# Performance work log

Measured on AMD Instinct MI355X. Metric: run time of the kernel, lower is better.

The kernel has to match this reference:

```python
import jax, jax.numpy as jnp
import numpy as np
import math

D_MODEL = 1024
N_HEADS = 16
D_K = D_MODEL // N_HEADS
B, S = 4, 2048


def setup_inputs() -> dict:
    key = jax.random.key(0)
    ks = jax.random.split(key, 11)
    std = 1.0 / math.sqrt(D_MODEL)
    inp = {
        "query": jax.random.normal(ks[0], (B, S, D_MODEL), dtype=jnp.float32),
        "key_in": jax.random.normal(ks[1], (B, S, D_MODEL), dtype=jnp.float32),
        "value": jax.random.normal(ks[2], (B, S, D_MODEL), dtype=jnp.float32),
        "Wq": jax.random.normal(ks[3], (D_MODEL, D_MODEL), dtype=jnp.float32) * std,
        "bq": jnp.zeros((D_MODEL,), dtype=jnp.float32),
        "Wk": jax.random.normal(ks[4], (D_MODEL, D_MODEL), dtype=jnp.float32) * std,
        "bk": jnp.zeros((D_MODEL,), dtype=jnp.float32),
        "Wv": jax.random.normal(ks[5], (D_MODEL, D_MODEL), dtype=jnp.float32) * std,
        "bv": jnp.zeros((D_MODEL,), dtype=jnp.float32),
        "Wo": jax.random.normal(ks[6], (D_MODEL, D_MODEL), dtype=jnp.float32) * std,
        "bo": jnp.zeros((D_MODEL,), dtype=jnp.float32),
    }
    return inp


def reference(query, key_in, value, Wq, bq, Wk, bk, Wv, bv, Wo, bo):
    b, s, _ = query.shape
    scale = math.sqrt(D_K)
    # projections: nn.Linear computes x @ W.T + b
    Q = (query @ Wq.T + bq).reshape(b, s, N_HEADS, D_K).transpose(0, 2, 1, 3)
    K = (key_in @ Wk.T + bk).reshape(b, s, N_HEADS, D_K).transpose(0, 2, 1, 3)
    V = (value @ Wv.T + bv).reshape(b, s, N_HEADS, D_K).transpose(0, 2, 1, 3)
    # [b, h, s, s]
    scores = jnp.einsum("bhqd,bhkd->bhqk", Q, K) / scale
    causal = jnp.tril(jnp.ones((s, s), dtype=bool))
    scores = jnp.where(causal[None, None, :, :], scores, jnp.float32(-1e9))
    attn = jax.nn.softmax(scores, axis=-1)
    out = jnp.einsum("bhqk,bhkd->bhqd", attn, V)
    out = out.transpose(0, 2, 1, 3).reshape(b, s, D_MODEL)
    return out @ Wo.T + bo
```

## Files before the change

### kernel.cpp

```cpp
#include <hip/hip_runtime.h>
#include <hip/hip_bf16.h>
#include <cstdint>

#define DM   1024
#define NH   16
#define DKK  64
#define BB   4
#define SS   2048

typedef __attribute__((ext_vector_type(8)))  short short8;
typedef __attribute__((ext_vector_type(4)))  float f32x4;
typedef __attribute__((ext_vector_type(16))) float f32x16;

__device__ __forceinline__ unsigned short f2bf(float f) {
    union { float f; uint32_t u; } v; v.f = f;
    uint32_t u = v.u;
    uint32_t r = (u + 0x7FFFu + ((u >> 16) & 1u)) >> 16;
    return (unsigned short)r;
}

#define GLL(src, dst) __builtin_amdgcn_global_load_lds(                      \
        (__attribute__((address_space(1))) void*)(src),                      \
        (__attribute__((address_space(3))) void*)(dst), 16, 0, 0)

__global__ void cvt_all(const float* __restrict__ q, const float* __restrict__ k,
                        const float* __restrict__ v,
                        const float* __restrict__ wq, const float* __restrict__ wk,
                        const float* __restrict__ wv, const float* __restrict__ wo,
                        unsigned short* __restrict__ dact, unsigned short* __restrict__ dw)
{
    int i = blockIdx.x * 256 + threadIdx.x;
    const float* s;
    unsigned short* d;
    if (i < 3145728) {
        int a = i >> 20, r = i & 1048575;
        int j = r >> 7, kb = r & 127;
        int kbs = (kb & ~7) | ((kb ^ j) & 7);
        s = (a == 0 ? q : a == 1 ? k : v) + (size_t)j * 1024 + kbs * 8;
        d = dact + ((size_t)a << 23) + (size_t)j * 1024 + kb * 8;
    } else {
        int t = i - 3145728;
        int a = t >> 17, r = t & 131071;
        int j = r >> 7, kb = r & 127;
        int kbs = (kb & ~7) | ((kb ^ j) & 7);
        s = (a == 0 ? wq : a == 1 ? wk : a == 2 ? wv : wo) + (size_t)j * 1024 + kbs * 8;
        d = dw + ((size_t)a << 20) + (size_t)j * 1024 + kb * 8;
    }
    float4 f0 = *(const float4*)(s);
    float4 f1 = *(const float4*)(s + 4);
    union { uint32_t u[4]; short8 s8; } c;
    asm("v_cvt_pk_bf16_f32 %0, %1, %2" : "=v"(c.u[0]) : "v"(f0.x), "v"(f0.y));
    asm("v_cvt_pk_bf16_f32 %0, %1, %2" : "=v"(c.u[1]) : "v"(f0.z), "v"(f0.w));
    asm("v_cvt_pk_bf16_f32 %0, %1, %2" : "=v"(c.u[2]) : "v"(f1.x), "v"(f1.y));
    asm("v_cvt_pk_bf16_f32 %0, %1, %2" : "=v"(c.u[3]) : "v"(f1.z), "v"(f1.w));
    *(short8*)d = c.s8;
}

__global__ __launch_bounds__(512, 2) void gemm_qkv(
        const unsigned short* __restrict__ Act,
        const unsigned short* __restrict__ Wq, const unsigned short* __restrict__ Wk,
        const unsigned short* __restrict__ Wv,
        const float* __restrict__ bq, const float* __restrict__ bk, const float* __restrict__ bv,
        unsigned short* __restrict__ Qo, unsigned short* __restrict__ Ko,
        unsigned short* __restrict__ Vo, const float qscale)
{
    const int orig = blockIdx.x;
    const int wid  = (orig & 7) * 48 + (orig >> 3);
    const int z    = wid >> 7;
    const int r    = wid & 127;
    const int brow = (r >> 2) * 256;
    const int bcol = (r & 3) * 256;

    const unsigned short* A  = Act + ((size_t)z << 23);
    const unsigned short* Bw = (z == 0) ? Wq : (z == 1) ? Wk : Wv;
    const float* bias        = (z == 0) ? bq : (z == 1) ? bk : bv;

    __shared__ __align__(16) unsigned short lA[2][2][8192];
    __shared__ __align__(16) unsigned short lB[2][2][8192];

    const int tid = threadIdx.x;
    const int w = tid >> 6, l = tid & 63;
    const int wm = w >> 2, wn = w & 3;
    const int lrow = l & 15, hi = l >> 4;

    const unsigned short* Asrc = A  + (size_t)(brow + (tid >> 3)) * 1024 + (tid & 7) * 8;
    const unsigned short* Bsrc = Bw + (size_t)(bcol + (tid >> 3)) * 1024 + (tid & 7) * 8;

    int axr[2];
    axr[0] = ((hi ^ (lrow & 7)) << 4);
    axr[1] = (((4 + hi) ^ (lrow & 7)) << 4);

    short8 bfr[4][2];
    f32x4 acc[8][4] = {};

#define STG_A(KT, H)                                                                         \
    { GLL(Asrc + (size_t)((H) * 128) * 1024 + (KT) * 64,      &lA[(KT) & 1][H][w * 512]);    \
      GLL(Asrc + (size_t)((H) * 128 + 64) * 1024 + (KT) * 64, &lA[(KT) & 1][H][4096 + w * 512]); }
#define STG_B(KT, H)                                                                         \
    { GLL(Bsrc + (size_t)((H) * 128) * 1024 + (KT) * 64,      &lB[(KT) & 1][H][w * 512]);    \
      GLL(Bsrc + (size_t)((H) * 128 + 64) * 1024 + (KT) * 64, &lB[(KT) & 1][H][4096 + w * 512]); }
#define VM4 asm volatile("s_waitcnt vmcnt(4)" ::: "memory")
#define VM0 asm volatile("s_waitcnt vmcnt(0)" ::: "memory")

#define PH(KT, MQ, READB, STG, WAIT)                                                         \
    {                                                                                        \
        const char* la_ = (const char*)lA[(KT) & 1][wm];                                     \
        const char* lb_ = (const char*)lB[(KT) & 1][wn >> 1];                                \
        if (READB) {                                                                         \
            _Pragma("unroll") for (int n = 0; n < 4; ++n)                                    \
            _Pragma("unroll") for (int kk = 0; kk < 2; ++kk)                                 \
                bfr[n][kk] = *(const short8*)(lb_ + ((wn & 1) * 64 + n * 16 + lrow) * 128 + axr[kk]); \
        }                                                                                    \
        short8 af_[2][2];                                                                    \
        _Pragma("unroll") for (int j = 0; j < 2; ++j)                                        \
        _Pragma("unroll") for (int kk = 0; kk < 2; ++kk)                                     \
            af_[j][kk] = *(const short8*)(la_ + (((MQ) * 2 + j) * 16 + lrow) * 128 + axr[kk]); \
        STG;                                                                                 \
        WAIT;                                                                                \
        __builtin_amdgcn_s_barrier();                                                        \
        asm volatile("s_waitcnt lgkmcnt(0)" ::: "memory");                                   \
        __builtin_amdgcn_sched_barrier(0);                                                   \
        __builtin_amdgcn_s_setprio(1);                                                       \
        _Pragma("unroll") for (int j = 0; j < 2; ++j)                                        \
        _Pragma("unroll") for (int n = 0; n < 4; ++n)                                        \
        _Pragma("unroll") for (int kk = 0; kk < 2; ++kk)                                     \
            acc[(MQ) * 2 + j][n] = __builtin_amdgcn_mfma_f32_16x16x32_bf16(                  \
                af_[j][kk], bfr[n][kk], acc[(MQ) * 2 + j][n], 0, 0, 0);                      \
        __builtin_amdgcn_s_setprio(0);                                                       \
        __builtin_amdgcn_s_barrier();                                                        \
    }

    STG_A(0, 0); STG_A(0, 1); STG_B(0, 0); STG_B(0, 1); STG_B(1, 0); STG_B(1, 1);
    VM4;
    __builtin_amdgcn_s_barrier();

    for (int i = 0; i < 7; ++i) {
        const int kt = 2 * i;
        PH(kt,     0, 1, STG_A(kt + 1, 0), (void)0);
        PH(kt,     1, 0, STG_A(kt + 1, 1), (void)0);
        PH(kt,     2, 0, STG_B(kt + 2, 0), (void)0);
        PH(kt,     3, 0, STG_B(kt + 2, 1), VM4);
        PH(kt + 1, 0, 1, STG_A(kt + 2, 0), (void)0);
        PH(kt + 1, 1, 0, STG_A(kt + 2, 1), (void)0);
        PH(kt + 1, 2, 0, STG_B(kt + 3, 0), (void)0);
        PH(kt + 1, 3, 0, STG_B(kt + 3, 1), VM4);
    }
    PH(14, 0, 1, STG_A(15, 0), (void)0);
    PH(14, 1, 0, STG_A(15, 1), (void)0);
    PH(14, 2, 0, (void)0, (void)0);
    PH(14, 3, 0, (void)0, VM0);
    PH(15, 0, 1, (void)0, (void)0);
    PH(15, 1, 0, (void)0, (void)0);
    PH(15, 2, 0, (void)0, (void)0);
    PH(15, 3, 0, (void)0, (void)0);

#undef PH
#undef STG_A
#undef STG_B

    const float ascale = (z == 0) ? qscale : 1.0f;
#pragma unroll
    for (int m = 0; m < 8; ++m) {
#pragma unroll
        for (int n = 0; n < 4; ++n) {
            const int i0 = brow + wm * 128 + m * 16 + hi * 4;
            const int j  = bcol + wn * 64 + n * 16 + lrow;
            const float bj = bias[j];
            const int hh = j >> 6, d = j & 63;
            if (z < 2) {
                unsigned short* Cb = (z == 0) ? Qo : Ko;
#pragma unroll
                for (int t = 0; t < 4; ++t) {
                    const int i = i0 + t;
                    const int b = i >> 11, s = i & 2047;
                    Cb[(((size_t)(b * NH + hh) * SS) + s) * DKK + d] = f2bf((acc[m][n][t] + bj) * ascale);
                }
            } else {
                const int b = i0 >> 11, s0 = i0 & 2047;
                ushort4 pk;
                pk.x = f2bf(acc[m][n][0] + bj);
                pk.y = f2bf(acc[m][n][1] + bj);
                pk.z = f2bf(acc[m][n][2] + bj);
                pk.w = f2bf(acc[m][n][3] + bj);
                *(ushort4*)(Vo + (((size_t)(b * NH + hh) * DKK) + d) * SS + s0) = pk;
            }
        }
    }
}

__global__ __launch_bounds__(256) void gemm_out(
        const unsigned short* __restrict__ A,
        const unsigned short* __restrict__ Bw,
        const float* __restrict__ bias,
        float* __restrict__ Cout)
{
    const int orig = blockIdx.y * 8 + blockIdx.x;
    const int wid  = (orig & 7) * 64 + (orig >> 3);
    const int brow = (wid >> 3) * 128;
    const int bcol = (wid & 7) * 128;

    __shared__ __align__(16) unsigned short lA[128 * 64];
    __shared__ __align__(16) unsigned short lB[2][128 * 64];

    const int tid = threadIdx.x;
    const int w = tid >> 6, l = tid & 63;
    const int wr = (w >> 1) * 64, wc = (w & 1) * 64;
    const int lrow = l & 15;
    const int hi = l >> 4;
    const int sr = l >> 3, scb = l & 7;

    const unsigned short* aga[4];
    const unsigned short* bga[4];
    int awb[4], lbo[4];
#pragma unroll
    for (int i = 0; i < 4; ++i) {
        const int chunk = w * 4 + i;
        const int r = chunk * 8 + sr;
        aga[i] = A  + (size_t)(brow + r) * 1024 + scb * 8;
        bga[i] = Bw + (size_t)(bcol + r) * 1024 + scb * 8;
        awb[i] = chunk * 1024 + sr * 128 + ((scb ^ sr) << 4);
        lbo[i] = chunk * 512;
    }

    short8 aX[4], aY[4];
    f32x4 acc[4][4] = {};

#pragma unroll
    for (int i = 0; i < 4; ++i) GLL(bga[i], lB[0] + lbo[i]);
#pragma unroll
    for (int i = 0; i < 4; ++i) aX[i] = *(const short8*)(aga[i]);
#pragma unroll
    for (int i = 0; i < 4; ++i) aY[i] = *(const short8*)(aga[i] + 64);

#define OUT_WR(CUR)                                                     \
    _Pragma("unroll")                                                   \
    for (int i = 0; i < 4; ++i)                                         \
        *(short8*)((char*)lA + awb[i]) = CUR[i];

#define OUT_MFMA(LB)                                                                              \
    {                                                                                             \
        const unsigned short* lb = (LB);                                                          \
        __builtin_amdgcn_s_setprio(1);                                                            \
        _Pragma("unroll")                                                                         \
        for (int kk = 0; kk < 2; ++kk) {                                                          \
            short8 af[4], bf[4];                                                                  \
            _Pragma("unroll")                                                                     \
            for (int m = 0; m < 4; ++m) {                                                         \
                const int row = wr + m * 16 + lrow;                                               \
                const int pb = (kk * 4 + hi) ^ (row & 7);                                         \
                af[m] = *(const short8*)((const char*)lA + row * 128 + (pb << 4));                \
            }                                                                                     \
            _Pragma("unroll")                                                                     \
            for (int n = 0; n < 4; ++n) {                                                         \
                const int row = wc + n * 16 + lrow;                                               \
                const int pb = (kk * 4 + hi) ^ (row & 7);                                         \
                bf[n] = *(const short8*)((const char*)lb + row * 128 + (pb << 4));                \
            }                                                                                     \
            _Pragma("unroll")                                                                     \
            for (int m = 0; m < 4; ++m)                                                           \
                _Pragma("unroll")                                                                 \
                for (int n = 0; n < 4; ++n)                                                       \
                    acc[m][n] = __builtin_amdgcn_mfma_f32_16x16x32_bf16(af[m], bf[n], acc[m][n], 0, 0, 0); \
        }                                                                                         \
        __builtin_amdgcn_s_setprio(0);                                                            \
    }

    for (int t = 0; t < 14; t += 2) {
        OUT_WR(aX);
        {
            const int ko = (t + 2) * 64;
#pragma unroll
            for (int i = 0; i < 4; ++i) aX[i] = *(const short8*)(aga[i] + ko);
            const int kb = (t + 1) * 64;
#pragma unroll
            for (int i = 0; i < 4; ++i) GLL(bga[i] + kb, lB[1] + lbo[i]);
        }
        asm volatile("s_waitcnt vmcnt(8) lgkmcnt(0)" ::: "memory");
        __builtin_amdgcn_s_barrier();
        OUT_MFMA(lB[0]);
        asm volatile("" ::: "memory");
        __builtin_amdgcn_s_barrier();

        OUT_WR(aY);
        {
            const int ko = (t + 3) * 64;
#pragma unroll
            for (int i = 0; i < 4; ++i) aY[i] = *(const short8*)(aga[i] + ko);
            const int kb = (t + 2) * 64;
#pragma unroll
            for (int i = 0; i < 4; ++i) GLL(bga[i] + kb, lB[0] + lbo[i]);
        }
        asm volatile("s_waitcnt vmcnt(8) lgkmcnt(0)" ::: "memory");
        __builtin_amdgcn_s_barrier();
        OUT_MFMA(lB[1]);
        asm volatile("" ::: "memory");
        __builtin_amdgcn_s_barrier();
    }
    OUT_WR(aX);
#pragma unroll
    for (int i = 0; i < 4; ++i) GLL(bga[i] + 15 * 64, lB[1] + lbo[i]);
    asm volatile("s_waitcnt vmcnt(4) lgkmcnt(0)" ::: "memory");
    __builtin_amdgcn_s_barrier();
    OUT_MFMA(lB[0]);
    asm volatile("" ::: "memory");
    __builtin_amdgcn_s_barrier();
    OUT_WR(aY);
    asm volatile("s_waitcnt vmcnt(0) lgkmcnt(0)" ::: "memory");
    __builtin_amdgcn_s_barrier();
    OUT_MFMA(lB[1]);

#pragma unroll
    for (int m = 0; m < 4; ++m) {
#pragma unroll
        for (int n = 0; n < 4; ++n) {
            const int i0 = brow + wr + m * 16 + (l >> 4) * 4;
            const int j  = bcol + wc + n * 16 + lrow;
            const float bj = bias[j];
#pragma unroll
            for (int t = 0; t < 4; ++t)
                Cout[(size_t)(i0 + t) * DM + j] = acc[m][n][t] + bj;
        }
    }
#undef OUT_WR
#undef OUT_MFMA
}

__global__ __launch_bounds__(256) void attn_kernel(
        const unsigned short* __restrict__ Q,
        const unsigned short* __restrict__ K,
        const unsigned short* __restrict__ Vt,
        unsigned short* __restrict__ AO)
{
    const int flat = blockIdx.y * 16 + blockIdx.x;
    const int r8 = flat & 7, k8 = flat >> 3;
    const int bh = r8 * 8 + (k8 & 7);
    const int qchunk = 15 - (k8 >> 3);
    const int tid = threadIdx.x;
    const int w = tid >> 6, l = tid & 63;
    const int ln = l & 31, h = l >> 5;
    const int qb = qchunk * 128;
    const int q0w = qb + w * 32;

    __shared__ __align__(16) char lK[2][4096];
    __shared__ __align__(16) char lV[2][4096];

    const unsigned short* Qp = Q  + ((size_t)bh * SS + q0w) * DKK;
    const unsigned short* Kp = K  + (size_t)bh * SS * DKK;
    const unsigned short* Vp = Vt + (size_t)bh * DKK * SS;

    const int srow = tid >> 3, scb = tid & 7;
    const int swb = srow * 128 + ((scb * 16) ^ ((srow & 7) << 4));
    const unsigned short* ksrc = Kp + srow * DKK + scb * 8;
    const int vd = (scb < 4) ? srow : (srow + 32);
    const unsigned short* vsrc = Vp + (size_t)vd * SS + (scb & 3) * 8;

    int ka[4], va[4];
#pragma unroll
    for (int ks = 0; ks < 4; ++ks)
        ka[ks] = ln * 128 + ((ks * 32 + h * 16) ^ ((ln & 7) << 4));
#pragma unroll
    for (int c = 0; c < 4; ++c)
        va[c] = ln * 128 + ((c * 32 + h * 16) ^ ((ln & 7) << 4));

    short8 qf[4];
#pragma unroll
    for (int ks = 0; ks < 4; ++ks)
        qf[ks] = *(const short8*)(Qp + (size_t)ln * DKK + ks * 16 + h * 8);

    f32x16 o0 = {}, o1 = {};
    float lsum = 0.f;

    const int Tc = qb / 32;
    const int NT = Tc + 4;

    auto compute = [&](int t, int buf) {
        const char* kb = lK[buf];
        const char* vb = lV[buf];
        short8 kf[4];
#pragma unroll
        for (int ks = 0; ks < 4; ++ks) kf[ks] = *(const short8*)(kb + ka[ks]);

        f32x16 s = {};
        __builtin_amdgcn_s_setprio(1);
#pragma unroll
        for (int ks = 0; ks < 4; ++ks)
            s = __builtin_amdgcn_mfma_f32_32x32x16_bf16(kf[ks], qf[ks], s, 0, 0, 0);
        __builtin_amdgcn_s_setprio(0);

        const bool diag = (t == Tc + w);
#pragma unroll
        for (int r = 0; r < 16; ++r) {
            float e;
            asm("v_exp_f32 %0, %1" : "=v"(e) : "v"(s[r]));
            if (diag) {
                const int crow = (r & 3) + 8 * (r >> 2) + 4 * h;
                e = (crow > ln) ? 0.f : e;
            }
            s[r] = e;
            lsum += e;
        }

        uint32_t pk[8];
#pragma unroll
        for (int i = 0; i < 8; ++i) {
            uint32_t d;
            asm("v_cvt_pk_bf16_f32 %0, %1, %2" : "=v"(d) : "v"(s[2 * i]), "v"(s[2 * i + 1]));
            pk[i] = d;
        }
        asm("v_permlane32_swap_b32 %0, %1" : "+v"(pk[0]), "+v"(pk[2]));
        asm("v_permlane32_swap_b32 %0, %1" : "+v"(pk[1]), "+v"(pk[3]));
        asm("v_permlane32_swap_b32 %0, %1" : "+v"(pk[4]), "+v"(pk[6]));
        asm("v_permlane32_swap_b32 %0, %1" : "+v"(pk[5]), "+v"(pk[7]));

        union Ux { uint32_t u[4]; short8 s8; } pa0, pa1;
        pa0.u[0] = pk[0]; pa0.u[1] = pk[1]; pa0.u[2] = pk[2]; pa0.u[3] = pk[3];
        pa1.u[0] = pk[4]; pa1.u[1] = pk[5]; pa1.u[2] = pk[6]; pa1.u[3] = pk[7];

        short8 vf00 = *(const short8*)(vb + va[0]);
        short8 vf10 = *(const short8*)(vb + va[1]);
        short8 vf01 = *(const short8*)(vb + va[2]);
        short8 vf11 = *(const short8*)(vb + va[3]);

        __builtin_amdgcn_s_setprio(1);
        o0 = __builtin_amdgcn_mfma_f32_32x32x16_bf16(pa0.s8, vf00, o0, 0, 0, 0);
        o0 = __builtin_amdgcn_mfma_f32_32x32x16_bf16(pa1.s8, vf10, o0, 0, 0, 0);
        o1 = __builtin_amdgcn_mfma_f32_32x32x16_bf16(pa0.s8, vf01, o1, 0, 0, 0);
        o1 = __builtin_amdgcn_mfma_f32_32x32x16_bf16(pa1.s8, vf11, o1, 0, 0, 0);
        __builtin_amdgcn_s_setprio(0);
    };

    short8 kA = *(const short8*)(ksrc);
    short8 vA = *(const short8*)(vsrc);
    *(short8*)(&lK[0][swb]) = kA;
    *(short8*)(&lV[0][swb]) = vA;
    kA = *(const short8*)(ksrc + 2048);
    vA = *(const short8*)(vsrc + 32);
    short8 kB = {}, vB = {};
    __syncthreads();

    int t = 0, buf = 0;
    for (;;) {
        if (t + 2 < NT) {
            kB = *(const short8*)(ksrc + (size_t)(t + 2) * 2048);
            vB = *(const short8*)(vsrc + (size_t)(t + 2) * 32);
        }
        if (t <= Tc + w) compute(t, buf);
        if (t + 1 < NT) {
            *(short8*)(&lK[buf ^ 1][swb]) = kA;
            *(short8*)(&lV[buf ^ 1][swb]) = vA;
        }
        __syncthreads();
        buf ^= 1;
        if (++t == NT) break;

        if (t + 2 < NT) {
            kA = *(const short8*)(ksrc + (size_t)(t + 2) * 2048);
            vA = *(const short8*)(vsrc + (size_t)(t + 2) * 32);
        }
        if (t <= Tc + w) compute(t, buf);
        if (t + 1 < NT) {
            *(short8*)(&lK[buf ^ 1][swb]) = kB;
            *(short8*)(&lV[buf ^ 1][swb]) = vB;
        }
        __syncthreads();
        buf ^= 1;
        if (++t == NT) break;
    }

    lsum += __shfl_xor(lsum, 32, 64);
    const float rcp = 1.0f / lsum;

    const int bb = bh >> 4, hh = bh & 15;
#pragma unroll
    for (int r = 0; r < 16; ++r) {
        const int crow = (r & 3) + 8 * (r >> 2) + 4 * h;
        const float rl = __shfl(rcp, crow, 64);
        const size_t row = (size_t)(bb * SS + q0w + crow) * DM + hh * DKK;
        AO[row + ln]      = f2bf(o0[r] * rl);
        AO[row + 32 + ln] = f2bf(o1[r] * rl);
    }
}

extern "C" void kernel_launch(void* const* d_in, const int* in_sizes, int n_in,
                              void* d_out, int out_size, void* d_ws, size_t ws_size,
                              hipStream_t stream)
{
    const float* query  = (const float*)d_in[0];
    const float* key_in = (const float*)d_in[1];
    const float* value  = (const float*)d_in[2];
    const float* Wq = (const float*)d_in[3];
    const float* bq = (const float*)d_in[4];
    const float* Wk = (const float*)d_in[5];
    const float* bk = (const float*)d_in[6];
    const float* Wv = (const float*)d_in[7];
    const float* bv = (const float*)d_in[8];
    const float* Wo = (const float*)d_in[9];
    const float* bo = (const float*)d_in[10];

    const size_t NACT = (size_t)BB * SS * DM;
    const size_t NWT  = (size_t)DM * DM;

    unsigned short* ws   = (unsigned short*)d_ws;
    unsigned short* actb = ws;
    unsigned short* wqb  = actb + 3 * NACT;
    unsigned short* wkb  = wqb + NWT;
    unsigned short* wvb  = wkb + NWT;
    unsigned short* wob  = wvb + NWT;
    unsigned short* Qb   = wob + NWT;
    unsigned short* Kb   = Qb + NACT;
    unsigned short* Vtb  = Kb + NACT;
    unsigned short* AOb  = Vtb + NACT;

    cvt_all<<<14336, 256, 0, stream>>>(query, key_in, value, Wq, Wk, Wv, Wo, actb, wqb);

    const float QSCALE = 0.125f * 1.44269504088896f;
    gemm_qkv<<<384, 512, 0, stream>>>(actb, wqb, wkb, wvb,
                                      bq, bk, bv, Qb, Kb, Vtb, QSCALE);

    attn_kernel<<<dim3(16, 64), 256, 0, stream>>>(Qb, Kb, Vtb, AOb);

    dim3 gg(DM / 128, (BB * SS) / 128);
    gemm_out<<<gg, 256, 0, stream>>>(AOb, wob, bo, (float*)d_out);
}
```

Measured before the change: 188.2 us.

## Fuse fp32-to-bf16 activation conversion into QKV GEMM A-tile loading

The separate conversion pass over the three fp32 activation tensors is removed. The QKV GEMM now loads fp32 activations into registers, converts them to bf16 in-kernel, and writes them to swizzled LDS, with register double-buffering (rX/rY) across k-steps. This avoids writing and re-reading about 48 MB of bf16 activations in global memory. In exchange it reads twice the A bytes inside the GEMM, adds register pressure and conversion ALU work, and replaces async global-to-LDS loads with register staging.

```diff
diff --git a/kernel.cpp b/kernel.cpp
--- a/kernel.cpp
+++ b/kernel.cpp
@@ -23,29 +23,16 @@
         (__attribute__((address_space(1))) void*)(src),                      \
         (__attribute__((address_space(3))) void*)(dst), 16, 0, 0)
 
-__global__ void cvt_all(const float* __restrict__ q, const float* __restrict__ k,
-                        const float* __restrict__ v,
-                        const float* __restrict__ wq, const float* __restrict__ wk,
-                        const float* __restrict__ wv, const float* __restrict__ wo,
-                        unsigned short* __restrict__ dact, unsigned short* __restrict__ dw)
+__global__ void cvt_w(const float* __restrict__ wq, const float* __restrict__ wk,
+                      const float* __restrict__ wv, const float* __restrict__ wo,
+                      unsigned short* __restrict__ dst)
 {
     int i = blockIdx.x * 256 + threadIdx.x;
-    const float* s;
-    unsigned short* d;
-    if (i < 3145728) {
-        int a = i >> 20, r = i & 1048575;
-        int j = r >> 7, kb = r & 127;
-        int kbs = (kb & ~7) | ((kb ^ j) & 7);
-        s = (a == 0 ? q : a == 1 ? k : v) + (size_t)j * 1024 + kbs * 8;
-        d = dact + ((size_t)a << 23) + (size_t)j * 1024 + kb * 8;
-    } else {
-        int t = i - 3145728;
-        int a = t >> 17, r = t & 131071;
-        int j = r >> 7, kb = r & 127;
-        int kbs = (kb & ~7) | ((kb ^ j) & 7);
-        s = (a == 0 ? wq : a == 1 ? wk : a == 2 ? wv : wo) + (size_t)j * 1024 + kbs * 8;
-        d = dw + ((size_t)a << 20) + (size_t)j * 1024 + kb * 8;
-    }
+    int a = i >> 17;
+    int r = i & 131071;
+    int j = r >> 7, kb = r & 127;
+    int kbs = (kb & ~7) | ((kb ^ j) & 7);
+    const float* s = (a == 0 ? wq : a == 1 ? wk : a == 2 ? wv : wo) + (size_t)j * 1024 + kbs * 8;
     float4 f0 = *(const float4*)(s);
     float4 f1 = *(const float4*)(s + 4);
     union { uint32_t u[4]; short8 s8; } c;
@@ -53,11 +40,11 @@
     asm("v_cvt_pk_bf16_f32 %0, %1, %2" : "=v"(c.u[1]) : "v"(f0.z), "v"(f0.w));
     asm("v_cvt_pk_bf16_f32 %0, %1, %2" : "=v"(c.u[2]) : "v"(f1.x), "v"(f1.y));
     asm("v_cvt_pk_bf16_f32 %0, %1, %2" : "=v"(c.u[3]) : "v"(f1.z), "v"(f1.w));
-    *(short8*)d = c.s8;
+    *(short8*)(dst + ((size_t)a << 20) + (size_t)j * 1024 + kb * 8) = c.s8;
 }
 
 __global__ __launch_bounds__(512, 2) void gemm_qkv(
-        const unsigned short* __restrict__ Act,
+        const float* __restrict__ Aq, const float* __restrict__ Ak, const float* __restrict__ Av,
         const unsigned short* __restrict__ Wq, const unsigned short* __restrict__ Wk,
         const unsigned short* __restrict__ Wv,
         const float* __restrict__ bq, const float* __restrict__ bk, const float* __restrict__ bv,
@@ -71,7 +58,7 @@
     const int brow = (r >> 2) * 256;
     const int bcol = (r & 3) * 256;
 
-    const unsigned short* A  = Act + ((size_t)z << 23);
+    const float* Af          = (z == 0) ? Aq : (z == 1) ? Ak : Av;
     const unsigned short* Bw = (z == 0) ? Wq : (z == 1) ? Wk : Wv;
     const float* bias        = (z == 0) ? bq : (z == 1) ? bk : bv;
 
@@ -83,7 +70,9 @@
     const int wm = w >> 2, wn = w & 3;
     const int lrow = l & 15, hi = l >> 4;
 
-    const unsigned short* Asrc = A  + (size_t)(brow + (tid >> 3)) * 1024 + (tid & 7) * 8;
+    const float* Asrcf = Af + (size_t)(brow + (tid >> 2)) * 1024 + (tid & 3) * 16;
+    const int arow = tid >> 2;
+    const int akb0 = (tid & 3) * 2;
     const unsigned short* Bsrc = Bw + (size_t)(bcol + (tid >> 3)) * 1024 + (tid & 7) * 8;
 
     int axr[2];
@@ -91,18 +80,34 @@
     axr[1] = (((4 + hi) ^ (lrow & 7)) << 4);
 
     short8 bfr[4][2];
+    f32x4 rX[8], rY[8];
     f32x4 acc[8][4] = {};
 
-#define STG_A(KT, H)                                                                         \
-    { GLL(Asrc + (size_t)((H) * 128) * 1024 + (KT) * 64,      &lA[(KT) & 1][H][w * 512]);    \
-      GLL(Asrc + (size_t)((H) * 128 + 64) * 1024 + (KT) * 64, &lA[(KT) & 1][H][4096 + w * 512]); }
+#define LOAD_A(KT, H, R)                                                                     \
+    { _Pragma("unroll") for (int i_ = 0; i_ < 4; ++i_)                                       \
+        R[(H) * 4 + i_] = *(const f32x4*)(Asrcf + (size_t)(H) * 131072 + (KT) * 64 + i_ * 4); }
+
+#define CVT_WR(R, KTW, H)                                                                    \
+    { _Pragma("unroll") for (int b_ = 0; b_ < 2; ++b_) {                                     \
+        union { uint32_t u[4]; short8 s8; } c_;                                              \
+        f32x4 a0_ = R[(H) * 4 + b_ * 2], a1_ = R[(H) * 4 + b_ * 2 + 1];                      \
+        asm("v_cvt_pk_bf16_f32 %0, %1, %2" : "=v"(c_.u[0]) : "v"(a0_[0]), "v"(a0_[1]));      \
+        asm("v_cvt_pk_bf16_f32 %0, %1, %2" : "=v"(c_.u[1]) : "v"(a0_[2]), "v"(a0_[3]));      \
+        asm("v_cvt_pk_bf16_f32 %0, %1, %2" : "=v"(c_.u[2]) : "v"(a1_[0]), "v"(a1_[1]));      \
+        asm("v_cvt_pk_bf16_f32 %0, %1, %2" : "=v"(c_.u[3]) : "v"(a1_[2]), "v"(a1_[3]));      \
+        const int kb_ = akb0 + b_;                                                           \
+        *(short8*)((char*)&lA[(KTW) & 1][H][0] + arow * 128 + ((kb_ << 4) ^ ((arow & 7) << 4))) = c_.s8; \
+    } }
+
 #define STG_B(KT, H)                                                                         \
     { GLL(Bsrc + (size_t)((H) * 128) * 1024 + (KT) * 64,      &lB[(KT) & 1][H][w * 512]);    \
       GLL(Bsrc + (size_t)((H) * 128 + 64) * 1024 + (KT) * 64, &lB[(KT) & 1][H][4096 + w * 512]); }
-#define VM4 asm volatile("s_waitcnt vmcnt(4)" ::: "memory")
-#define VM0 asm volatile("s_waitcnt vmcnt(0)" ::: "memory")
-
-#define PH(KT, MQ, READB, STG, WAIT)                                                         \
+
+#define LGKM0 asm volatile("s_waitcnt lgkmcnt(0)" ::: "memory")
+#define VM12  asm volatile("s_waitcnt vmcnt(12)" ::: "memory")
+#define VM0   asm volatile("s_waitcnt vmcnt(0)" ::: "memory")
+
+#define PH(KT, MQ, READB, STG, CVTWR, WAIT)                                                  \
     {                                                                                        \
         const char* la_ = (const char*)lA[(KT) & 1][wm];                                     \
         const char* lb_ = (const char*)lB[(KT) & 1][wn >> 1];                                \
@@ -116,6 +121,7 @@
         _Pragma("unroll") for (int kk = 0; kk < 2; ++kk)                                     \
             af_[j][kk] = *(const short8*)(la_ + (((MQ) * 2 + j) * 16 + lrow) * 128 + axr[kk]); \
         STG;                                                                                 \
+        CVTWR;                                                                               \
         WAIT;                                                                                \
         __builtin_amdgcn_s_barrier();                                                        \
         asm volatile("s_waitcnt lgkmcnt(0)" ::: "memory");                                   \
@@ -130,33 +136,38 @@
         __builtin_amdgcn_s_barrier();                                                        \
     }
 
-    STG_A(0, 0); STG_A(0, 1); STG_B(0, 0); STG_B(0, 1); STG_B(1, 0); STG_B(1, 1);
-    VM4;
+    LOAD_A(0, 0, rX); LOAD_A(0, 1, rX);
+    STG_B(0, 0); STG_B(0, 1);
+    LOAD_A(1, 0, rY); LOAD_A(1, 1, rY);
+    STG_B(1, 0); STG_B(1, 1);
+    CVT_WR(rX, 0, 0); CVT_WR(rX, 0, 1);
+    asm volatile("s_waitcnt vmcnt(12) lgkmcnt(0)" ::: "memory");
     __builtin_amdgcn_s_barrier();
 
     for (int i = 0; i < 7; ++i) {
         const int kt = 2 * i;
-        PH(kt,     0, 1, STG_A(kt + 1, 0), (void)0);
-        PH(kt,     1, 0, STG_A(kt + 1, 1), (void)0);
-        PH(kt,     2, 0, STG_B(kt + 2, 0), (void)0);
-        PH(kt,     3, 0, STG_B(kt + 2, 1), VM4);
-        PH(kt + 1, 0, 1, STG_A(kt + 2, 0), (void)0);
-        PH(kt + 1, 1, 0, STG_A(kt + 2, 1), (void)0);
-        PH(kt + 1, 2, 0, STG_B(kt + 3, 0), (void)0);
-        PH(kt + 1, 3, 0, STG_B(kt + 3, 1), VM4);
-    }
-    PH(14, 0, 1, STG_A(15, 0), (void)0);
-    PH(14, 1, 0, STG_A(15, 1), (void)0);
-    PH(14, 2, 0, (void)0, (void)0);
-    PH(14, 3, 0, (void)0, VM0);
-    PH(15, 0, 1, (void)0, (void)0);
-    PH(15, 1, 0, (void)0, (void)0);
-    PH(15, 2, 0, (void)0, (void)0);
-    PH(15, 3, 0, (void)0, (void)0);
+        PH(kt,     0, 1, LOAD_A(kt + 2, 0, rX), CVT_WR(rY, kt + 1, 0), LGKM0);
+        PH(kt,     1, 0, LOAD_A(kt + 2, 1, rX), CVT_WR(rY, kt + 1, 1), LGKM0);
+        PH(kt,     2, 0, STG_B(kt + 2, 0),      (void)0,               (void)0);
+        PH(kt,     3, 0, STG_B(kt + 2, 1),      (void)0,               VM12);
+        PH(kt + 1, 0, 1, LOAD_A(kt + 3, 0, rY), CVT_WR(rX, kt + 2, 0), LGKM0);
+        PH(kt + 1, 1, 0, LOAD_A(kt + 3, 1, rY), CVT_WR(rX, kt + 2, 1), LGKM0);
+        PH(kt + 1, 2, 0, STG_B(kt + 3, 0),      (void)0,               (void)0);
+        PH(kt + 1, 3, 0, STG_B(kt + 3, 1),      (void)0,               VM12);
+    }
+    PH(14, 0, 1, (void)0, CVT_WR(rY, 15, 0), LGKM0);
+    PH(14, 1, 0, (void)0, CVT_WR(rY, 15, 1), LGKM0);
+    PH(14, 2, 0, (void)0, (void)0,           (void)0);
+    PH(14, 3, 0, (void)0, (void)0,           VM0);
+    PH(15, 0, 1, (void)0, (void)0,           (void)0);
+    PH(15, 1, 0, (void)0, (void)0,           (void)0);
+    PH(15, 2, 0, (void)0, (void)0,           (void)0);
+    PH(15, 3, 0, (void)0, (void)0,           (void)0);
 
 #undef PH
-#undef STG_A
 #undef STG_B
+#undef LOAD_A
+#undef CVT_WR
 
     const float ascale = (z == 0) ? qscale : 1.0f;
 #pragma unroll
@@ -500,21 +511,20 @@
     const size_t NACT = (size_t)BB * SS * DM;
     const size_t NWT  = (size_t)DM * DM;
 
-    unsigned short* ws   = (unsigned short*)d_ws;
-    unsigned short* actb = ws;
-    unsigned short* wqb  = actb + 3 * NACT;
-    unsigned short* wkb  = wqb + NWT;
-    unsigned short* wvb  = wkb + NWT;
-    unsigned short* wob  = wvb + NWT;
-    unsigned short* Qb   = wob + NWT;
-    unsigned short* Kb   = Qb + NACT;
-    unsigned short* Vtb  = Kb + NACT;
-    unsigned short* AOb  = Vtb + NACT;
-
-    cvt_all<<<14336, 256, 0, stream>>>(query, key_in, value, Wq, Wk, Wv, Wo, actb, wqb);
+    unsigned short* ws  = (unsigned short*)d_ws;
+    unsigned short* wqb = ws;
+    unsigned short* wkb = wqb + NWT;
+    unsigned short* wvb = wkb + NWT;
+    unsigned short* wob = wvb + NWT;
+    unsigned short* Qb  = wob + NWT;
+    unsigned short* Kb  = Qb + NACT;
+    unsigned short* Vtb = Kb + NACT;
+    unsigned short* AOb = Vtb + NACT;
+
+    cvt_w<<<2048, 256, 0, stream>>>(Wq, Wk, Wv, Wo, ws);
 
     const float QSCALE = 0.125f * 1.44269504088896f;
-    gemm_qkv<<<384, 512, 0, stream>>>(actb, wqb, wkb, wvb,
+    gemm_qkv<<<384, 512, 0, stream>>>(query, key_in, value, wqb, wkb, wvb,
                                       bq, bk, bv, Qb, Kb, Vtb, QSCALE);
 
     attn_kernel<<<dim3(16, 64), 256, 0, stream>>>(Qb, Kb, Vtb, AOb);
```

Result: faster. 179.3 us (-4.7%).
